# Optimization experiments

Hardware: AMD Instinct MI355X
Metric: run time of the kernel (lower is better)

The kernel has to match this reference:

```python
import jax, jax.numpy as jnp
import numpy as np

EMBED_DIM = 1024
NUM_HEADS = 16
HEAD_DIM = EMBED_DIM // NUM_HEADS


def setup_inputs() -> dict:
    key = jax.random.key(0)
    ks = jax.random.split(key, 10)
    s = 1.0 / np.sqrt(EMBED_DIM)
    inp = {
        "x1": jax.random.normal(ks[0], (4, 1024, EMBED_DIM), jnp.float32),
        "x2": jax.random.normal(ks[1], (4, 2048, EMBED_DIM), jnp.float32),
        "Wq": jax.random.normal(ks[2], (EMBED_DIM, EMBED_DIM), jnp.float32) * s,
        "bq": jnp.zeros((EMBED_DIM,), jnp.float32),
        "Wk": jax.random.normal(ks[3], (EMBED_DIM, EMBED_DIM), jnp.float32) * s,
        "bk": jnp.zeros((EMBED_DIM,), jnp.float32),
        "Wv": jax.random.normal(ks[4], (EMBED_DIM, EMBED_DIM), jnp.float32) * s,
        "bv": jnp.zeros((EMBED_DIM,), jnp.float32),
        "Wo": jax.random.normal(ks[5], (EMBED_DIM, EMBED_DIM), jnp.float32) * s,
        "bo": jnp.zeros((EMBED_DIM,), jnp.float32),
    }
    return inp


def reference(x1, x2, Wq, bq, Wk, bk, Wv, bv, Wo, bo):
    B, Sq, E = x1.shape
    Skv = x2.shape[1]
    H, D = NUM_HEADS, HEAD_DIM
    # linear projections (PyTorch Linear: x @ W.T + b)
    q = (x1 @ Wq.T + bq).reshape(B, Sq, H, D).transpose(0, 2, 1, 3)   # [B,H,Sq,D]
    k = (x2 @ Wk.T + bk).reshape(B, Skv, H, D).transpose(0, 2, 1, 3)  # [B,H,Skv,D]
    v = (x2 @ Wv.T + bv).reshape(B, Skv, H, D).transpose(0, 2, 1, 3)
    scores = jnp.einsum("bhqd,bhkd->bhqk", q, k) / jnp.sqrt(jnp.float32(D))
    attn = jax.nn.softmax(scores, axis=-1)
    out = jnp.einsum("bhqk,bhkd->bhqd", attn, v)
    out = out.transpose(0, 2, 1, 3).reshape(B, Sq, E)
    return out @ Wo.T + bo
```

## Files before the change

### kernel.cpp

```cpp
#include <hip/hip_runtime.h>

typedef __attribute__((ext_vector_type(8))) short short8;
typedef __attribute__((ext_vector_type(4))) short short4v;
typedef __attribute__((ext_vector_type(4))) float f32x4;
typedef _Float16 half8 __attribute__((ext_vector_type(8)));

#define ASYNC16(g, l) __builtin_amdgcn_global_load_lds( \
    (__attribute__((address_space(1))) void*)(g), \
    (__attribute__((address_space(3))) void*)(l), 16, 0, 0)

__device__ __forceinline__ short f2bf(float f) {
  union { float f; unsigned u; } v; v.f = f;
  unsigned r = v.u + 0x7fffu + ((v.u >> 16) & 1u);
  return (short)(r >> 16);
}

__device__ __forceinline__ short f2h(float f) {
  _Float16 h = (_Float16)f;
  return __builtin_bit_cast(short, h);
}

__device__ __forceinline__ unsigned pkh2(float a, float b) {
  return __builtin_bit_cast(unsigned, __builtin_amdgcn_cvt_pkrtz(a, b));
}

__device__ __forceinline__ f32x4 fzero4() {
  f32x4 z; z[0] = 0.f; z[1] = 0.f; z[2] = 0.f; z[3] = 0.f; return z;
}

__device__ __forceinline__ void wg_barrier() {
  asm volatile("s_waitcnt lgkmcnt(0)\n\ts_barrier" ::: "memory");
}

__global__ __launch_bounds__(256) void cvt_all(
    const float* __restrict__ x1, const float* __restrict__ x2,
    const float* __restrict__ wq, const float* __restrict__ wk,
    const float* __restrict__ wv, const float* __restrict__ wo,
    short* __restrict__ dst) {
  long e = ((long)blockIdx.x * 256 + threadIdx.x) * 4;
  const float* src; long loc;
  if (e < 4194304L)       { src = x1; loc = e; }
  else if (e < 12582912L) { src = x2; loc = e - 4194304L; }
  else if (e < 13631488L) { src = wq; loc = e - 12582912L; }
  else if (e < 14680064L) { src = wk; loc = e - 13631488L; }
  else if (e < 15728640L) { src = wv; loc = e - 14680064L; }
  else                    { src = wo; loc = e - 15728640L; }
  float4 v = *(const float4*)(src + loc);
  short4v o;
  o[0] = f2bf(v.x); o[1] = f2bf(v.y); o[2] = f2bf(v.z); o[3] = f2bf(v.w);
  *(short4v*)(dst + e) = o;
}

__global__ __launch_bounds__(256) void proj(
    const short* __restrict__ xb1, const short* __restrict__ xb2,
    const short* __restrict__ wqp, const short* __restrict__ wkp, const short* __restrict__ wvp,
    const float* __restrict__ bq, const float* __restrict__ bk, const float* __restrict__ bv,
    short* __restrict__ qb, short* __restrict__ kb, short* __restrict__ vb) {
  __shared__ short smem[16384];
  short* As = smem;
  short* Bs = smem + 4096;
  const int tid = threadIdx.x, w = tid >> 6, lane = tid & 63;
  const int quad = lane >> 4, col = lane & 15;
  const int waveM = (w >> 1) * 64, waveN = (w & 1) * 64;
  const int my = blockIdx.x, bn = blockIdx.y * 128;
  const short* A; const short* W; const float* bias; int mode, bm;
  if (my < 32)      { A = xb1; W = wqp; bias = bq; mode = 0; bm = my * 128; }
  else if (my < 96) { A = xb2; W = wkp; bias = bk; mode = 1; bm = (my - 32) * 128; }
  else              { A = xb2; W = wvp; bias = bv; mode = 2; bm = (my - 96) * 128; }

  f32x4 acc[4][4];
  for (int mi = 0; mi < 4; ++mi)
    for (int ni = 0; ni < 4; ++ni)
      acc[mi][ni] = fzero4();

  const int srow = w * 16 + (lane >> 2), scol = (lane & 3) * 8;
  const short* ga = A + (size_t)(bm + srow) * 1024 + scol;
  const short* gb = W + (size_t)(bn + srow) * 1024 + scol;
  short* lA = As + w * 512;
  short* lB = Bs + w * 512;

  for (int kk = 0; kk < 1024; kk += 32) {
    __syncthreads();
    ASYNC16(ga + kk,         lA);
    ASYNC16(ga + kk + 65536, lA + 2048);
    ASYNC16(gb + kk,         lB);
    ASYNC16(gb + kk + 65536, lB + 2048);
    __syncthreads();
    short8 af[4], bf[4];
    for (int mi = 0; mi < 4; ++mi)
      af[mi] = *(const short8*)(As + (waveM + mi * 16 + col) * 32 + quad * 8);
    for (int ni = 0; ni < 4; ++ni)
      bf[ni] = *(const short8*)(Bs + (waveN + ni * 16 + col) * 32 + quad * 8);
    for (int mi = 0; mi < 4; ++mi)
      for (int ni = 0; ni < 4; ++ni)
        acc[mi][ni] = __builtin_amdgcn_mfma_f32_16x16x32_bf16(af[mi], bf[ni], acc[mi][ni], 0, 0, 0);
  }

  __syncthreads();
  for (int ni = 0; ni < 4; ++ni) {
    int nn = waveN + ni * 16 + col;
    float bvl = bias[bn + nn];
    for (int mi = 0; mi < 4; ++mi) {
      int m0 = waveM + mi * 16 + quad * 4;
      for (int r = 0; r < 4; ++r) {
        int m = m0 + r;
        float val = acc[mi][ni][r] + bvl;
        short sv;
        if (mode == 0)      sv = f2bf(val * 0.18033688011112042f);
        else if (mode == 1) sv = f2bf(val);
        else                sv = f2h(val);
        smem[m * 128 + (nn ^ ((m & 15) << 3))] = sv;
      }
    }
  }
  __syncthreads();
  if (mode < 2) {
    const int S = (mode == 0) ? 1024 : 2048;
    short* outp = (mode == 0) ? qb : kb;
    const int bb = bm / S, s0 = bm & (S - 1), h0 = bn >> 6;
    for (int it = 0; it < 8; ++it) {
      int f = (it * 256 + tid) * 8;
      int hh = f >> 13, rem = f & 8191, m = rem >> 6, d = rem & 63;
      int nn = hh * 64 + d;
      short8 val = *(const short8*)&smem[m * 128 + (nn ^ ((m & 15) << 3))];
      *(short8*)(outp + ((((size_t)(bb * 16 + h0 + hh)) * S + s0 + m) * 64 + d)) = val;
    }
  } else {
    const int bb = bm >> 11, s0 = bm & 2047, kt0 = s0 >> 6, h0 = bn >> 6;
    for (int it = 0; it < 8; ++it) {
      int f = (it * 256 + tid) * 8;
      int hh = f >> 13, rem = f & 8191, ktl = rem >> 12, r3 = rem & 4095;
      int d = r3 >> 6, kvp0 = r3 & 63;
      int nn = hh * 64 + d;
      short8 val;
      for (int j = 0; j < 8; ++j) {
        int kvp = kvp0 + j;
        int kv = ((kvp & 3) << 4) | (kvp >> 2);
        int m = ktl * 64 + kv;
        val[j] = smem[m * 128 + (nn ^ ((m & 15) << 3))];
      }
      *(short8*)(vb + ((((size_t)(bb * 16 + h0 + hh)) * 32 + (kt0 + ktl)) * 4096) + d * 64 + kvp0) = val;
    }
  }
}

__global__ __launch_bounds__(256) void out_gemm(
    const short* __restrict__ A, const short* __restrict__ W,
    const float* __restrict__ bias, float* __restrict__ out) {
  __shared__ short As[2][4096];
  __shared__ short Bs[2][2048];
  const int tid = threadIdx.x, w = tid >> 6, lane = tid & 63;
  const int quad = lane >> 4, col = lane & 15;
  const int waveM = (w >> 1) * 64, waveN = (w & 1) * 32;
  const int bn = blockIdx.x * 64, bm = blockIdx.y * 128;

  f32x4 acc[4][2];
  for (int mi = 0; mi < 4; ++mi)
    for (int ni = 0; ni < 2; ++ni)
      acc[mi][ni] = fzero4();

  const int arow = w * 16 + (lane >> 2), ac = (lane & 3) * 8;
  const short* ga = A + (size_t)(bm + arow) * 1024 + ac;
  const short* gb = W + (size_t)(bn + (tid >> 2)) * 1024 + (tid & 3) * 8;
  short* lA0 = As[0] + w * 512; short* lA1 = As[1] + w * 512;
  short* lB0 = Bs[0] + w * 512; short* lB1 = Bs[1] + w * 512;

  for (int kk = 0; kk < 1024; kk += 64) {
    __syncthreads();
    ASYNC16(ga + kk,              lA0);
    ASYNC16(ga + kk + 65536,      lA0 + 2048);
    ASYNC16(ga + kk + 32,         lA1);
    ASYNC16(ga + kk + 32 + 65536, lA1 + 2048);
    ASYNC16(gb + kk,              lB0);
    ASYNC16(gb + kk + 32,         lB1);
    __syncthreads();
    for (int kh = 0; kh < 2; ++kh) {
      const short* Ash = As[kh];
      const short* Bsh = Bs[kh];
      short8 af[4], bf[2];
      for (int mi = 0; mi < 4; ++mi)
        af[mi] = *(const short8*)(Ash + (waveM + mi * 16 + col) * 32 + quad * 8);
      for (int ni = 0; ni < 2; ++ni)
        bf[ni] = *(const short8*)(Bsh + (waveN + ni * 16 + col) * 32 + quad * 8);
      for (int mi = 0; mi < 4; ++mi)
        for (int ni = 0; ni < 2; ++ni)
          acc[mi][ni] = __builtin_amdgcn_mfma_f32_16x16x32_bf16(af[mi], bf[ni], acc[mi][ni], 0, 0, 0);
    }
  }

  for (int ni = 0; ni < 2; ++ni) {
    int n = bn + waveN + ni * 16 + col;
    float bvl = bias[n];
    for (int mi = 0; mi < 4; ++mi) {
      int m0 = bm + waveM + mi * 16 + quad * 4;
      for (int r = 0; r < 4; ++r)
        out[(size_t)(m0 + r) * 1024 + n] = acc[mi][ni][r] + bvl;
    }
  }
}

__global__ __launch_bounds__(256, 2) void attn(
    const short* __restrict__ Q, const short* __restrict__ K,
    const short* __restrict__ V, short* __restrict__ O) {
  __shared__ short Ks[128 * 72];
  __shared__ short Vs[80 * 136];
  __shared__ short Ps[128 * 136];
  const int tid = threadIdx.x, w = tid >> 6, lane = tid & 63;
  const int quad = lane >> 4, col = lane & 15;
  const int bh = blockIdx.x, qt = blockIdx.y;
  const int b = bh >> 4, h = bh & 15;
  const int qbase = w * 32;

  const short* qp = Q + ((size_t)bh * 1024 + qt * 128) * 64;
  const short* kp = K + (size_t)bh * 131072;
  const short* vp = V + (size_t)bh * 131072;

  short8 aq[2][2];
  for (int mi = 0; mi < 2; ++mi) {
    const short* qr = qp + (qbase + mi * 16 + col) * 64 + quad * 8;
    aq[mi][0] = *(const short8*)qr;
    aq[mi][1] = *(const short8*)(qr + 32);
  }

  f32x4 oa[2][5];
  for (int mi = 0; mi < 2; ++mi)
    for (int ni = 0; ni < 5; ++ni)
      oa[mi][ni] = fzero4();

  for (int i = tid; i < 16 * 136; i += 256)
    Vs[64 * 136 + i] = (i < 136) ? (short)0x3C00 : (short)0;

  const int krow = lane + (w >> 1) * 64, kch = (w & 1) * 32;
  const int vd = lane, vch = w & 1, vkh = (w >> 1) * 32;

  short8 kpre[4], vpre[4];
  {
    const short* kg = kp + krow * 64 + kch;
    const short* vg = vp + vch * 4096 + vd * 64 + vkh;
    for (int i = 0; i < 4; ++i) kpre[i] = *(const short8*)(kg + i * 8);
    for (int i = 0; i < 4; ++i) vpre[i] = *(const short8*)(vg + i * 8);
  }

  for (int kt = 0; kt < 16; ++kt) {
    wg_barrier();
    for (int i = 0; i < 4; ++i)
      *(short8*)&Ks[krow * 72 + kch + i * 8] = kpre[i];
    for (int i = 0; i < 4; ++i)
      *(short8*)&Vs[vd * 136 + vch * 64 + vkh + i * 8] = vpre[i];
    {
      int ktn = (kt < 15) ? kt + 1 : kt;
      const short* kg = kp + ktn * 8192 + krow * 64 + kch;
      const short* vg = vp + (2 * ktn + vch) * 4096 + vd * 64 + vkh;
      for (int i = 0; i < 4; ++i) kpre[i] = *(const short8*)(kg + i * 8);
      for (int i = 0; i < 4; ++i) vpre[i] = *(const short8*)(vg + i * 8);
    }
    wg_barrier();

    f32x4 sf[2][8];
    for (int nk = 0; nk < 8; ++nk) {
      short8 bk0 = *(const short8*)&Ks[(nk * 16 + col) * 72 + quad * 8];
      short8 bk1 = *(const short8*)&Ks[(nk * 16 + col) * 72 + 32 + quad * 8];
      f32x4 z0 = fzero4(), z1 = fzero4();
      z0 = __builtin_amdgcn_mfma_f32_16x16x32_bf16(aq[0][0], bk0, z0, 0, 0, 0);
      z0 = __builtin_amdgcn_mfma_f32_16x16x32_bf16(aq[0][1], bk1, z0, 0, 0, 0);
      z1 = __builtin_amdgcn_mfma_f32_16x16x32_bf16(aq[1][0], bk0, z1, 0, 0, 0);
      z1 = __builtin_amdgcn_mfma_f32_16x16x32_bf16(aq[1][1], bk1, z1, 0, 0, 0);
      sf[0][nk] = z0;
      sf[1][nk] = z1;
    }

    for (int mi = 0; mi < 2; ++mi)
      for (int nk = 0; nk < 8; ++nk)
        for (int r = 0; r < 4; ++r)
          sf[mi][nk][r] = __builtin_amdgcn_exp2f(sf[mi][nk][r]);
    for (int mi = 0; mi < 2; ++mi)
      for (int r = 0; r < 4; ++r) {
        int row = qbase + mi * 16 + quad * 4 + r;
        uint2 d0, d1;
        d0.x = pkh2(sf[mi][0][r], sf[mi][1][r]);
        d0.y = pkh2(sf[mi][2][r], sf[mi][3][r]);
        d1.x = pkh2(sf[mi][4][r], sf[mi][5][r]);
        d1.y = pkh2(sf[mi][6][r], sf[mi][7][r]);
        *(uint2*)&Ps[row * 136 + col * 4]      = d0;
        *(uint2*)&Ps[row * 136 + 64 + col * 4] = d1;
      }

    for (int ks = 0; ks < 4; ++ks) {
      int koff = ks * 32 + quad * 8;
      half8 ap0 = *(const half8*)&Ps[(qbase + col) * 136 + koff];
      half8 ap1 = *(const half8*)&Ps[(qbase + 16 + col) * 136 + koff];
      for (int ni = 0; ni < 5; ++ni) {
        half8 bv = *(const half8*)&Vs[(ni * 16 + col) * 136 + koff];
        oa[0][ni] = __builtin_amdgcn_mfma_f32_16x16x32_f16(ap0, bv, oa[0][ni], 0, 0, 0);
        oa[1][ni] = __builtin_amdgcn_mfma_f32_16x16x32_f16(ap1, bv, oa[1][ni], 0, 0, 0);
      }
    }
  }

  float inv[2][4];
  for (int mi = 0; mi < 2; ++mi)
    for (int r = 0; r < 4; ++r) {
      float s = __shfl(oa[mi][4][r], lane & 48);
      inv[mi][r] = 1.f / s;
    }
  __syncthreads();
  for (int mi = 0; mi < 2; ++mi)
    for (int ni = 0; ni < 4; ++ni)
      for (int r = 0; r < 4; ++r)
        Ps[(qbase + mi * 16 + quad * 4 + r) * 64 + ni * 16 + col] = f2bf(oa[mi][ni][r] * inv[mi][r]);
  __syncthreads();
  for (int it = 0; it < 4; ++it) {
    int f = (it * 256 + tid) * 8;
    int q = f >> 6, d = f & 63;
    short8 val = *(const short8*)&Ps[q * 64 + d];
    *(short8*)(O + ((size_t)(b * 1024 + qt * 128 + q)) * 1024 + h * 64 + d) = val;
  }
}

extern "C" void kernel_launch(void* const* d_in, const int* in_sizes, int n_in,
                              void* d_out, int out_size, void* d_ws, size_t ws_size,
                              hipStream_t stream) {
  const float* x1 = (const float*)d_in[0];
  const float* x2 = (const float*)d_in[1];
  const float* Wq = (const float*)d_in[2];
  const float* bq = (const float*)d_in[3];
  const float* Wk = (const float*)d_in[4];
  const float* bk = (const float*)d_in[5];
  const float* Wv = (const float*)d_in[6];
  const float* bv = (const float*)d_in[7];
  const float* Wo = (const float*)d_in[8];
  const float* bo = (const float*)d_in[9];

  char* ws = (char*)d_ws;
  short* xb1 = (short*)(ws + 0);
  short* xb2 = (short*)(ws + 8388608);
  short* wqb = (short*)(ws + 25165824);
  short* wkb = (short*)(ws + 27262976);
  short* wvb = (short*)(ws + 29360128);
  short* wob = (short*)(ws + 31457280);
  short* qb  = (short*)(ws + 33554432);
  short* kb  = (short*)(ws + 41943040);
  short* vb  = (short*)(ws + 58720256);
  short* ob  = (short*)(ws + 75497472);

  cvt_all<<<16384, 256, 0, stream>>>(x1, x2, Wq, Wk, Wv, Wo, (short*)ws);
  proj<<<dim3(160, 8), 256, 0, stream>>>(xb1, xb2, wqb, wkb, wvb, bq, bk, bv, qb, kb, vb);
  attn<<<dim3(64, 8), 256, 0, stream>>>(qb, kb, vb, ob);
  out_gemm<<<dim3(16, 32), 256, 0, stream>>>(ob, wob, bo, (float*)d_out);
}
```

Measured before the change: 242.6 us.

## Double-buffer LDS tiles in projection and output GEMMs to overlap loads with MFMA

Both the QKV projection GEMM and the output GEMM now use two LDS buffers. Async global-to-LDS loads for the next k-tile are issued before the MFMA compute on the current tile, and a combined vmcnt/lgkmcnt barrier is used. The aim is to hide global load latency behind matrix math and drop one barrier per step. In exchange, the out_gemm LDS footprint doubles, and the projection buffers now overlap the epilogue smem region, which could lower occupancy.

```diff
diff --git a/kernel.cpp b/kernel.cpp
--- a/kernel.cpp
+++ b/kernel.cpp
@@ -30,6 +30,10 @@
 
 __device__ __forceinline__ void wg_barrier() {
   asm volatile("s_waitcnt lgkmcnt(0)\n\ts_barrier" ::: "memory");
+}
+
+__device__ __forceinline__ void pipe_barrier() {
+  asm volatile("s_waitcnt vmcnt(0) lgkmcnt(0)\n\ts_barrier" ::: "memory");
 }
 
 __global__ __launch_bounds__(256) void cvt_all(
@@ -57,8 +61,6 @@
     const float* __restrict__ bq, const float* __restrict__ bk, const float* __restrict__ bv,
     short* __restrict__ qb, short* __restrict__ kb, short* __restrict__ vb) {
   __shared__ short smem[16384];
-  short* As = smem;
-  short* Bs = smem + 4096;
   const int tid = threadIdx.x, w = tid >> 6, lane = tid & 63;
   const int quad = lane >> 4, col = lane & 15;
   const int waveM = (w >> 1) * 64, waveN = (w & 1) * 64;
@@ -76,27 +78,39 @@
   const int srow = w * 16 + (lane >> 2), scol = (lane & 3) * 8;
   const short* ga = A + (size_t)(bm + srow) * 1024 + scol;
   const short* gb = W + (size_t)(bn + srow) * 1024 + scol;
-  short* lA = As + w * 512;
-  short* lB = Bs + w * 512;
-
-  for (int kk = 0; kk < 1024; kk += 32) {
-    __syncthreads();
+
+  auto stage = [&](int b, int kk) {
+    short* lA = smem + b * 8192 + w * 512;
+    short* lB = smem + b * 8192 + 4096 + w * 512;
     ASYNC16(ga + kk,         lA);
     ASYNC16(ga + kk + 65536, lA + 2048);
     ASYNC16(gb + kk,         lB);
     ASYNC16(gb + kk + 65536, lB + 2048);
-    __syncthreads();
+  };
+  auto compute = [&](int b) {
+    const short* As_ = smem + b * 8192;
+    const short* Bs_ = As_ + 4096;
     short8 af[4], bf[4];
     for (int mi = 0; mi < 4; ++mi)
-      af[mi] = *(const short8*)(As + (waveM + mi * 16 + col) * 32 + quad * 8);
+      af[mi] = *(const short8*)(As_ + (waveM + mi * 16 + col) * 32 + quad * 8);
     for (int ni = 0; ni < 4; ++ni)
-      bf[ni] = *(const short8*)(Bs + (waveN + ni * 16 + col) * 32 + quad * 8);
+      bf[ni] = *(const short8*)(Bs_ + (waveN + ni * 16 + col) * 32 + quad * 8);
     for (int mi = 0; mi < 4; ++mi)
       for (int ni = 0; ni < 4; ++ni)
         acc[mi][ni] = __builtin_amdgcn_mfma_f32_16x16x32_bf16(af[mi], bf[ni], acc[mi][ni], 0, 0, 0);
-  }
-
-  __syncthreads();
+  };
+
+  stage(0, 0);
+  pipe_barrier();
+  for (int it = 0; it < 16; ++it) {
+    stage(1, it * 64 + 32);
+    compute(0);
+    pipe_barrier();
+    if (it < 15) stage(0, it * 64 + 64);
+    compute(1);
+    pipe_barrier();
+  }
+
   for (int ni = 0; ni < 4; ++ni) {
     int nn = waveN + ni * 16 + col;
     float bvl = bias[bn + nn];
@@ -147,8 +161,7 @@
 __global__ __launch_bounds__(256) void out_gemm(
     const short* __restrict__ A, const short* __restrict__ W,
     const float* __restrict__ bias, float* __restrict__ out) {
-  __shared__ short As[2][4096];
-  __shared__ short Bs[2][2048];
+  __shared__ short smem[24576];
   const int tid = threadIdx.x, w = tid >> 6, lane = tid & 63;
   const int quad = lane >> 4, col = lane & 15;
   const int waveM = (w >> 1) * 64, waveN = (w & 1) * 32;
@@ -162,21 +175,25 @@
   const int arow = w * 16 + (lane >> 2), ac = (lane & 3) * 8;
   const short* ga = A + (size_t)(bm + arow) * 1024 + ac;
   const short* gb = W + (size_t)(bn + (tid >> 2)) * 1024 + (tid & 3) * 8;
-  short* lA0 = As[0] + w * 512; short* lA1 = As[1] + w * 512;
-  short* lB0 = Bs[0] + w * 512; short* lB1 = Bs[1] + w * 512;
-
-  for (int kk = 0; kk < 1024; kk += 64) {
-    __syncthreads();
+
+  auto stage = [&](int b, int kk) {
+    short* base = smem + b * 12288;
+    short* lA0 = base + w * 512;
+    short* lA1 = base + 4096 + w * 512;
+    short* lB0 = base + 8192 + w * 512;
+    short* lB1 = base + 10240 + w * 512;
     ASYNC16(ga + kk,              lA0);
     ASYNC16(ga + kk + 65536,      lA0 + 2048);
     ASYNC16(ga + kk + 32,         lA1);
     ASYNC16(ga + kk + 32 + 65536, lA1 + 2048);
     ASYNC16(gb + kk,              lB0);
     ASYNC16(gb + kk + 32,         lB1);
-    __syncthreads();
+  };
+  auto compute = [&](int b) {
+    const short* base = smem + b * 12288;
     for (int kh = 0; kh < 2; ++kh) {
-      const short* Ash = As[kh];
-      const short* Bsh = Bs[kh];
+      const short* Ash = base + kh * 4096;
+      const short* Bsh = base + 8192 + kh * 2048;
       short8 af[4], bf[2];
       for (int mi = 0; mi < 4; ++mi)
         af[mi] = *(const short8*)(Ash + (waveM + mi * 16 + col) * 32 + quad * 8);
@@ -186,6 +203,17 @@
         for (int ni = 0; ni < 2; ++ni)
           acc[mi][ni] = __builtin_amdgcn_mfma_f32_16x16x32_bf16(af[mi], bf[ni], acc[mi][ni], 0, 0, 0);
     }
+  };
+
+  stage(0, 0);
+  pipe_barrier();
+  for (int it = 0; it < 8; ++it) {
+    stage(1, it * 128 + 64);
+    compute(0);
+    pipe_barrier();
+    if (it < 7) stage(0, it * 128 + 128);
+    compute(1);
+    pipe_barrier();
   }
 
   for (int ni = 0; ni < 2; ++ni) {
```

Result: no change. 239.4 us (-1.3%).
